# Performance work log

Measured on AMD Instinct MI355X. Metric: run time of the kernel, lower is better.

Reference implementation:

```python
import math
import jax, jax.numpy as jnp
import numpy as np

V = 32000   # vocab_size
NL = 8      # n_layer
NH = 16     # n_head
D = 1024    # n_embd
DH = D // NH
FF = 4 * D
B = 2
L = 1024
EPS = 1e-5


def setup_inputs() -> dict:
    key = jax.random.key(0)
    ks = jax.random.split(key, 10)
    std = 0.02  # matches nn.init.normal_(std=0.02)
    def nrm(k, shape):
        return jax.random.normal(k, shape, jnp.float32) * std
    return {
        "idx": jax.random.randint(ks[0], (B, L), 0, V),
        "tok_emb": nrm(ks[1], (V, D)),
        # per-layer params stacked on leading NL axis (scanned over)
        "ln1_w": jnp.ones((NL, D)), "ln1_b": jnp.zeros((NL, D)),
        "wq": nrm(ks[2], (NL, D, D)), "wk": nrm(ks[3], (NL, D, D)),
        "wv": nrm(ks[4], (NL, D, D)), "wo": nrm(ks[5], (NL, D, D)),
        "ln2_w": jnp.ones((NL, D)), "ln2_b": jnp.zeros((NL, D)),
        "w1": nrm(ks[6], (NL, D, FF)), "b1": jnp.zeros((NL, FF)),
        "w2": nrm(ks[7], (NL, FF, D)), "b2": jnp.zeros((NL, D)),
        "lnf_w": jnp.ones((D,)), "lnf_b": jnp.zeros((D,)),
        "lm_head": nrm(ks[8], (D, V)),
    }


def _sinusoidal_pe(seq_len, dim):
    pos = jnp.arange(seq_len, dtype=jnp.float32)[:, None]
    div = jnp.exp(jnp.arange(0, dim, 2, dtype=jnp.float32) * (-math.log(10000.0) / dim))
    pe = jnp.zeros((seq_len, dim), jnp.float32)
    pe = pe.at[:, 0::2].set(jnp.sin(pos * div))
    pe = pe.at[:, 1::2].set(jnp.cos(pos * div))
    return pe


def _ln(x, w, b):
    m = x.mean(-1, keepdims=True)
    v = ((x - m) ** 2).mean(-1, keepdims=True)
    return (x - m) * jax.lax.rsqrt(v + EPS) * w + b


def reference(idx, tok_emb, ln1_w, ln1_b, wq, wk, wv, wo,
              ln2_w, ln2_b, w1, b1, w2, b2, lnf_w, lnf_b, lm_head):
    b, l = idx.shape
    x = tok_emb[idx] + _sinusoidal_pe(l, tok_emb.shape[1])[None]  # [B,L,D]
    causal = jnp.tril(jnp.ones((l, l), bool))
    scale = 1.0 / math.sqrt(DH)

    def block(x, p):
        l1w, l1b, Wq, Wk, Wv, Wo, l2w, l2b, W1, B1, W2, B2 = p
        h = _ln(x, l1w, l1b)
        def heads(W):  # [B,L,D] -> [B,H,L,DH]
            return (h @ W).reshape(b, l, NH, DH).transpose(0, 2, 1, 3)
        q, k, v = heads(Wq), heads(Wk), heads(Wv)
        att = jnp.einsum('bhqd,bhkd->bhqk', q, k) * scale
        att = jnp.where(causal, att, -jnp.inf)
        att = jax.nn.softmax(att, axis=-1)
        y = jnp.einsum('bhqk,bhkd->bhqd', att, v)
        y = y.transpose(0, 2, 1, 3).reshape(b, l, -1)
        x = x + y @ Wo
        h2 = _ln(x, l2w, l2b)
        x = x + jax.nn.gelu(h2 @ W1 + B1, approximate=False) @ W2 + B2
        return x, None

    x, _ = jax.lax.scan(
        block, x, (ln1_w, ln1_b, wq, wk, wv, wo, ln2_w, ln2_b, w1, b1, w2, b2))
    x = _ln(x, lnf_w, lnf_b)
    return x @ lm_head  # [B,L,V] logits
```

## Files before the change

kernel.cpp:

```cpp
#include <hip/hip_runtime.h>
#include <math.h>

typedef unsigned short u16;
typedef __bf16 bfx8 __attribute__((ext_vector_type(8)));
typedef float f32x4 __attribute__((ext_vector_type(4)));

#define NLAYER  8
#define NHEAD   16
#define DMODEL  1024
#define DHEAD   64
#define DFF     4096
#define NB      2
#define SEQ     1024
#define NVOCAB  32000
#define NTOK    (NB*SEQ)
#define EPSLN   1e-5f
#define VCHUNK  6400
#define NSPLIT  2

__device__ __forceinline__ float bf2f(u16 u) {
  union { unsigned int i; float f; } x; x.i = ((unsigned int)u) << 16; return x.f;
}
__device__ __forceinline__ u16 f2bf(float f) {
  unsigned int x = __float_as_uint(f);
  x += 0x7fffu + ((x >> 16) & 1u);
  return (u16)(x >> 16);
}

#if defined(__has_builtin)
#if __has_builtin(__builtin_amdgcn_global_load_lds)
#define HAVE_GLL 1
#endif
#endif

__device__ __forceinline__ void gll16(const void* g, void* lds_base, int lane) {
#ifdef HAVE_GLL
  __builtin_amdgcn_global_load_lds((const __attribute__((address_space(1))) unsigned int*)g,
                                   (__attribute__((address_space(3))) unsigned int*)lds_base,
                                   16, 0, 0);
  (void)lane;
#else
  *(uint4*)((char*)lds_base + lane * 16) = *(const uint4*)g;
#endif
}

enum { EPI_QKV = 0, EPI_GELU_BIAS = 1, EPI_RESID = 2, EPI_RESID_BIAS = 3, EPI_LOGITS = 4 };

template <int EPI, int BM>
__global__ __launch_bounds__(256) void gemm_bt(
    const u16* __restrict__ A, const u16* __restrict__ Bt,
    const float* __restrict__ bias, u16* __restrict__ outb,
    float* __restrict__ outf, int M, int N, int K, int ldc)
{
  constexpr int ARND = BM / 32;
  constexpr int MF = BM / 32;
  constexpr int ABYTES = BM * 64 * 2;
  constexpr int BBYTES = 128 * 64 * 2;
  __shared__ __align__(16) u16 sA[2][BM * 64];
  __shared__ __align__(16) u16 sB[2][128 * 64];

  const int tid  = threadIdx.x;
  const int w    = tid >> 6;
  const int lane = tid & 63;
  const int l16  = lane & 15;
  const int hi   = lane >> 4;
  const int wm   = w >> 1;
  const int wn   = w & 1;

  const int nwg = gridDim.x;
  const int MB  = M / BM;
  const int orig = blockIdx.x;
  const int xcd = orig & 7, li = orig >> 3;
  const int q = nwg >> 3, r = nwg & 7;
  const int work = (xcd < r ? xcd * (q + 1) : r * (q + 1) + (xcd - r) * q) + li;
  const int m0 = (work % MB) * BM;
  const int n0 = (work / MB) * 128;

  const int srow8 = lane >> 3;
  const int su    = lane & 7;

  const u16* gA[ARND]; const u16* gB[4];
  int laOff[ARND]; int lbOff[4];
#pragma unroll
  for (int r2 = 0; r2 < ARND; r2++) {
    const int row = r2 * 32 + w * 8 + srow8;
    const int gu = su ^ (row & 7);
    gA[r2] = A + (size_t)(m0 + row) * K + gu * 8;
    laOff[r2] = (r2 * 32 + w * 8) * 128;
  }
#pragma unroll
  for (int r2 = 0; r2 < 4; r2++) {
    const int row = r2 * 32 + w * 8 + srow8;
    const int gu = su ^ (row & 7);
    gB[r2] = Bt + (size_t)(n0 + row) * K + gu * 8;
    lbOff[r2] = (r2 * 32 + w * 8) * 128;
  }

  f32x4 acc[MF][4];
#pragma unroll
  for (int i = 0; i < MF; i++)
#pragma unroll
    for (int j = 0; j < 4; j++)
#pragma unroll
      for (int r2 = 0; r2 < 4; r2++) acc[i][j][r2] = 0.0f;

#pragma unroll
  for (int r2 = 0; r2 < ARND; r2++) { gll16(gA[r2], (char*)sA[0] + laOff[r2], lane); gA[r2] += 64; }
#pragma unroll
  for (int r2 = 0; r2 < 4; r2++)    { gll16(gB[r2], (char*)sB[0] + lbOff[r2], lane); gB[r2] += 64; }
  __syncthreads();

  const int NT = K >> 6;
  int cur = 0;
  for (int t = 0; t < NT; ++t) {
    if (t + 1 < NT) {
      char* nA = (char*)sA[0] + (cur ^ 1) * ABYTES;
      char* nB = (char*)sB[0] + (cur ^ 1) * BBYTES;
#pragma unroll
      for (int r2 = 0; r2 < ARND; r2++) { gll16(gA[r2], nA + laOff[r2], lane); gA[r2] += 64; }
#pragma unroll
      for (int r2 = 0; r2 < 4; r2++)    { gll16(gB[r2], nB + lbOff[r2], lane); gB[r2] += 64; }
    }

    const char* cA = (const char*)sA[0] + cur * ABYTES;
    const char* cB = (const char*)sB[0] + cur * BBYTES;
    bfx8 aF[MF][2], bF[4][2];
#pragma unroll
    for (int i = 0; i < MF; i++) {
      const int row = wm * (BM / 2) + i * 16 + l16;
      const int rsw = row & 7;
#pragma unroll
      for (int kk = 0; kk < 2; kk++)
        aF[i][kk] = *(const bfx8*)(cA + row * 128 + ((kk * 4 + hi) ^ rsw) * 16);
    }
#pragma unroll
    for (int j = 0; j < 4; j++) {
      const int row = wn * 64 + j * 16 + l16;
      const int rsw = row & 7;
#pragma unroll
      for (int kk = 0; kk < 2; kk++)
        bF[j][kk] = *(const bfx8*)(cB + row * 128 + ((kk * 4 + hi) ^ rsw) * 16);
    }
#pragma unroll
    for (int kk = 0; kk < 2; kk++)
#pragma unroll
      for (int i = 0; i < MF; i++)
#pragma unroll
        for (int j = 0; j < 4; j++)
          acc[i][j] = __builtin_amdgcn_mfma_f32_16x16x32_bf16(aF[i][kk], bF[j][kk], acc[i][j], 0, 0, 0);
    __syncthreads();
    cur ^= 1;
  }

  const int rbase = m0 + wm * (BM / 2);
  const int cbase = n0 + wn * 64;
#pragma unroll
  for (int i = 0; i < MF; i++) {
#pragma unroll
    for (int j = 0; j < 4; j++) {
      const int gcol = cbase + j * 16 + l16;
      float bv = 0.0f;
      if constexpr (EPI == EPI_GELU_BIAS || EPI == EPI_RESID_BIAS) bv = bias[gcol];
#pragma unroll
      for (int r2 = 0; r2 < 4; r2++) {
        const int grow = rbase + i * 16 + hi * 4 + r2;
        float v = acc[i][j][r2];
        const size_t oi = (size_t)grow * ldc + gcol;
        if constexpr (EPI == EPI_QKV) {
          outb[oi] = f2bf(v);
        } else if constexpr (EPI == EPI_GELU_BIAS) {
          v += bv;
          v = 0.5f * v * (1.0f + erff(v * 0.70710678118654752f));
          outb[oi] = f2bf(v);
        } else if constexpr (EPI == EPI_RESID) {
          outf[oi] += v;
        } else if constexpr (EPI == EPI_RESID_BIAS) {
          outf[oi] += v + bv;
        } else {
          outf[oi] = v;
        }
      }
    }
  }
}

__global__ __launch_bounds__(256) void ln_kernel(
    const float* __restrict__ x, const float* __restrict__ w,
    const float* __restrict__ b, u16* __restrict__ out)
{
  const int row = blockIdx.x;
  const int tid = threadIdx.x;
  const float* xr = x + (size_t)row * DMODEL;
  float4 v = *(const float4*)(xr + tid * 4);
  __shared__ float sbuf[4];
  float s = v.x + v.y + v.z + v.w;
#pragma unroll
  for (int o = 32; o > 0; o >>= 1) s += __shfl_xor(s, o, 64);
  if ((tid & 63) == 0) sbuf[tid >> 6] = s;
  __syncthreads();
  const float mean = (sbuf[0] + sbuf[1] + sbuf[2] + sbuf[3]) * (1.0f / DMODEL);
  __syncthreads();
  float d0 = v.x - mean, d1 = v.y - mean, d2 = v.z - mean, d3 = v.w - mean;
  float qq = d0 * d0 + d1 * d1 + d2 * d2 + d3 * d3;
#pragma unroll
  for (int o = 32; o > 0; o >>= 1) qq += __shfl_xor(qq, o, 64);
  if ((tid & 63) == 0) sbuf[tid >> 6] = qq;
  __syncthreads();
  const float var = (sbuf[0] + sbuf[1] + sbuf[2] + sbuf[3]) * (1.0f / DMODEL);
  const float rstd = rsqrtf(var + EPSLN);
  const int c = tid * 4;
  float dv[4] = {d0, d1, d2, d3};
#pragma unroll
  for (int e = 0; e < 4; e++)
    out[(size_t)row * DMODEL + c + e] = f2bf(dv[e] * rstd * w[c + e] + b[c + e]);
}

__global__ __launch_bounds__(256) void embed_kernel(
    const int* __restrict__ idx, const float* __restrict__ tok, float* __restrict__ x)
{
  const int row = blockIdx.x;
  const int l = row & (SEQ - 1);
  const int t = idx[row];
  const int d = threadIdx.x * 4;
#pragma unroll
  for (int e = 0; e < 4; e++) {
    const int dd = d + e;
    const float freq = expf((float)(dd & ~1) * (-9.210340371976184f / (float)DMODEL));
    const float ang = (float)l * freq;
    const float pe = (dd & 1) ? cosf(ang) : sinf(ang);
    x[(size_t)row * DMODEL + dd] = tok[(size_t)t * DMODEL + dd] + pe;
  }
}

__global__ __launch_bounds__(256) void transpose_b(
    const float* __restrict__ in0, u16* __restrict__ out0, int rows, int cols,
    size_t in_ls, size_t out_ls)
{
  __shared__ float tile[32][33];
  const float* in = in0 + (size_t)blockIdx.z * in_ls;
  u16* out = out0 + (size_t)blockIdx.z * out_ls;
  const int c0 = blockIdx.x * 32, r0 = blockIdx.y * 32;
  const int tx = threadIdx.x & 31, ty = threadIdx.x >> 5;
#pragma unroll
  for (int i = ty; i < 32; i += 8)
    tile[i][tx] = in[(size_t)(r0 + i) * cols + c0 + tx];
  __syncthreads();
#pragma unroll
  for (int i = ty; i < 32; i += 8)
    out[(size_t)(c0 + i) * rows + r0 + tx] = f2bf(tile[tx][i]);
}

__global__ __launch_bounds__(256) void transpose6_kernel(
    const float* __restrict__ wq, const float* __restrict__ wk,
    const float* __restrict__ wv, const float* __restrict__ wo,
    const float* __restrict__ w1, const float* __restrict__ w2,
    u16* __restrict__ wT)
{
  __shared__ float tile[32][33];
  const size_t dd = (size_t)DMODEL * DMODEL, dff = (size_t)DMODEL * DFF;
  const int t = blockIdx.x;
  const float* in; u16* out; int rows, cols, cx, cy;
  if (t < 4096) {
    const int mat = t >> 10, tl = t & 1023;
    in = (mat == 0) ? wq : (mat == 1) ? wk : (mat == 2) ? wv : wo;
    out = wT + (size_t)mat * dd; rows = DMODEL; cols = DMODEL;
    cx = tl & 31; cy = tl >> 5;
  } else if (t < 8192) {
    const int tl = t - 4096;
    in = w1; out = wT + 4 * dd; rows = DMODEL; cols = DFF;
    cx = tl & 127; cy = tl >> 7;
  } else {
    const int tl = t - 8192;
    in = w2; out = wT + 4 * dd + dff; rows = DFF; cols = DMODEL;
    cx = tl & 31; cy = tl >> 5;
  }
  const int c0 = cx * 32, r0 = cy * 32;
  const int tx = threadIdx.x & 31, ty = threadIdx.x >> 5;
#pragma unroll
  for (int i = ty; i < 32; i += 8)
    tile[i][tx] = in[(size_t)(r0 + i) * cols + c0 + tx];
  __syncthreads();
#pragma unroll
  for (int i = ty; i < 32; i += 8)
    out[(size_t)(c0 + i) * rows + r0 + tx] = f2bf(tile[tx][i]);
}

__global__ __launch_bounds__(256) void vtrans_kernel(
    const u16* __restrict__ qkv, u16* __restrict__ vt)
{
  __shared__ u16 tile[32][33];
  const int bh = blockIdx.z;
  const int b = bh >> 4, hh = bh & 15;
  const int l0 = blockIdx.x * 32, d0 = blockIdx.y * 32;
  const int tx = threadIdx.x & 31, ty = threadIdx.x >> 5;
#pragma unroll
  for (int i = ty; i < 32; i += 8)
    tile[i][tx] = qkv[(size_t)(b * SEQ + l0 + i) * (3 * DMODEL) + 2 * DMODEL + hh * DHEAD + d0 + tx];
  __syncthreads();
#pragma unroll
  for (int i = ty; i < 32; i += 8)
    vt[(size_t)(bh * DHEAD + d0 + i) * SEQ + l0 + tx] = tile[tx][i];
}

__device__ __forceinline__ int plds_byte(int row, int col) {
  return row * 128 + ((((col >> 3) ^ (row & 7)) << 3) + (col & 7)) * 2;
}

__global__ __launch_bounds__(64) void attn_partial(
    const u16* __restrict__ qkv, const u16* __restrict__ vt,
    float* __restrict__ opart, float* __restrict__ lpart)
{
  __shared__ __align__(16) u16 p_lds[32 * 64];
  const int lane = threadIdx.x;
  const int l16 = lane & 15, hi = lane >> 4;
  const int qt = blockIdx.x, hh = blockIdx.y;
  const int b = blockIdx.z >> 1, sp = blockIdx.z & 1;
  const int q0 = qt * 32;
  const int T = (q0 + 95) >> 6;
  const int t_lo = (T * sp) >> 1;
  const int t_hi = (T * (sp + 1)) >> 1;

  const u16* qptr = qkv;
  const u16* kptr = qkv + DMODEL;
  const size_t rs3 = 3 * DMODEL;
  const size_t hoff = (size_t)hh * DHEAD;

  bfx8 aQ[2][2];
#pragma unroll
  for (int mt = 0; mt < 2; mt++)
#pragma unroll
    for (int kf = 0; kf < 2; kf++)
      aQ[mt][kf] = *(const bfx8*)&qptr[(size_t)(b * SEQ + q0 + mt * 16 + l16) * rs3 + hoff + kf * 32 + hi * 8];

  f32x4 o[2][4];
  float ssum[2][4];
#pragma unroll
  for (int mt = 0; mt < 2; mt++)
#pragma unroll
    for (int r = 0; r < 4; r++) ssum[mt][r] = 0.0f;
#pragma unroll
  for (int mt = 0; mt < 2; mt++)
#pragma unroll
    for (int dt = 0; dt < 4; dt++)
#pragma unroll
      for (int r = 0; r < 4; r++) o[mt][dt][r] = 0.0f;

  for (int kt = t_lo; kt < t_hi; kt++) {
    const int k0 = kt * 64;
    const bool diag = (kt == T - 1);

    bfx8 bK[4][2];
#pragma unroll
    for (int nt = 0; nt < 4; nt++)
#pragma unroll
      for (int kf = 0; kf < 2; kf++)
        bK[nt][kf] = *(const bfx8*)&kptr[(size_t)(b * SEQ + k0 + nt * 16 + l16) * rs3 + hoff + kf * 32 + hi * 8];

    f32x4 s[2][4];
#pragma unroll
    for (int mt = 0; mt < 2; mt++)
#pragma unroll
      for (int nt = 0; nt < 4; nt++) {
#pragma unroll
        for (int r = 0; r < 4; r++) s[mt][nt][r] = 0.0f;
        s[mt][nt] = __builtin_amdgcn_mfma_f32_16x16x32_bf16(aQ[mt][0], bK[nt][0], s[mt][nt], 0, 0, 0);
        s[mt][nt] = __builtin_amdgcn_mfma_f32_16x16x32_bf16(aQ[mt][1], bK[nt][1], s[mt][nt], 0, 0, 0);
      }

#pragma unroll
    for (int mt = 0; mt < 2; mt++) {
#pragma unroll
      for (int r = 0; r < 4; r++) {
        const int row_l = mt * 16 + hi * 4 + r;
        const int qrow = q0 + row_l;
        float p[4], rsum = 0.0f;
#pragma unroll
        for (int nt = 0; nt < 4; nt++) {
          const float sv = s[mt][nt][r] * 0.125f;
          const bool mask = diag && (k0 + nt * 16 + l16 > qrow);
          p[nt] = mask ? 0.0f : __expf(sv);
          rsum += p[nt];
        }
#pragma unroll
        for (int t = 1; t < 16; t <<= 1) rsum += __shfl_xor(rsum, t, 64);
        ssum[mt][r] += rsum;
#pragma unroll
        for (int nt = 0; nt < 4; nt++)
          *(u16*)((char*)p_lds + plds_byte(row_l, nt * 16 + l16)) = f2bf(p[nt]);
      }
    }
    __syncthreads();

    bfx8 pa[2][2];
#pragma unroll
    for (int mt = 0; mt < 2; mt++) {
      const int row = mt * 16 + l16;
#pragma unroll
      for (int kf = 0; kf < 2; kf++)
        pa[mt][kf] = *(const bfx8*)((const char*)p_lds + row * 128 + (((kf * 4 + hi) ^ (row & 7)) << 4));
    }
    bfx8 bV[4][2];
    const size_t vbase = (size_t)(b * NHEAD + hh) * DHEAD * SEQ;
#pragma unroll
    for (int dt = 0; dt < 4; dt++)
#pragma unroll
      for (int kf = 0; kf < 2; kf++)
        bV[dt][kf] = *(const bfx8*)&vt[vbase + (size_t)(dt * 16 + l16) * SEQ + k0 + kf * 32 + hi * 8];
#pragma unroll
    for (int mt = 0; mt < 2; mt++)
#pragma unroll
      for (int dt = 0; dt < 4; dt++) {
        o[mt][dt] = __builtin_amdgcn_mfma_f32_16x16x32_bf16(pa[mt][0], bV[dt][0], o[mt][dt], 0, 0, 0);
        o[mt][dt] = __builtin_amdgcn_mfma_f32_16x16x32_bf16(pa[mt][1], bV[dt][1], o[mt][dt], 0, 0, 0);
      }
    __syncthreads();
  }

  const size_t pbase = (((size_t)sp * NB + b) * NHEAD + hh) * SEQ + q0;
#pragma unroll
  for (int mt = 0; mt < 2; mt++) {
#pragma unroll
    for (int r = 0; r < 4; r++) {
      const int row_l = mt * 16 + hi * 4 + r;
      const size_t rg = pbase + row_l;
      if (l16 == 0) lpart[rg] = ssum[mt][r];
#pragma unroll
      for (int dt = 0; dt < 4; dt++)
        opart[rg * DHEAD + dt * 16 + l16] = o[mt][dt][r];
    }
  }
}

__global__ __launch_bounds__(256) void attn_combine(
    const float* __restrict__ opart, const float* __restrict__ lpart,
    u16* __restrict__ y)
{
  const int row = blockIdx.x;
  const int b = row >> 10;
  const int l = row & (SEQ - 1);
  const int t = threadIdx.x;
  const int hh = t >> 4;
  const int d0 = (t & 15) * 4;
  const size_t base = ((size_t)b * NHEAD + hh) * SEQ + l;
  const size_t stride = (size_t)NB * NHEAD * SEQ;
  float wsum = 0.0f;
  float4 acc = make_float4(0.f, 0.f, 0.f, 0.f);
#pragma unroll
  for (int i = 0; i < NSPLIT; i++) {
    wsum += lpart[base + i * stride];
    const float4 ov = *(const float4*)&opart[(base + i * stride) * DHEAD + d0];
    acc.x += ov.x; acc.y += ov.y; acc.z += ov.z; acc.w += ov.w;
  }
  const float dn = 1.0f / wsum;
  u16* yp = y + (size_t)row * DMODEL + hh * DHEAD + d0;
  yp[0] = f2bf(acc.x * dn);
  yp[1] = f2bf(acc.y * dn);
  yp[2] = f2bf(acc.z * dn);
  yp[3] = f2bf(acc.w * dn);
}

extern "C" void kernel_launch(void* const* d_in, const int* in_sizes, int n_in,
                              void* d_out, int out_size, void* d_ws, size_t ws_size,
                              hipStream_t stream)
{
  (void)in_sizes; (void)n_in; (void)out_size;
  const int*   idx  = (const int*)d_in[0];
  const float* tok  = (const float*)d_in[1];
  const float* ln1w = (const float*)d_in[2];
  const float* ln1b = (const float*)d_in[3];
  const float* wq   = (const float*)d_in[4];
  const float* wk   = (const float*)d_in[5];
  const float* wv   = (const float*)d_in[6];
  const float* wo   = (const float*)d_in[7];
  const float* ln2w = (const float*)d_in[8];
  const float* ln2b = (const float*)d_in[9];
  const float* w1   = (const float*)d_in[10];
  const float* b1   = (const float*)d_in[11];
  const float* w2   = (const float*)d_in[12];
  const float* b2   = (const float*)d_in[13];
  const float* lnfw = (const float*)d_in[14];
  const float* lnfb = (const float*)d_in[15];
  const float* lmh  = (const float*)d_in[16];
  float* out = (float*)d_out;

  char* ws = (char*)d_ws;
  size_t off = 0;
  auto alloc = [&](size_t bytes) -> void* {
    void* p = ws + off;
    off += (bytes + 255) & ~(size_t)255;
    return p;
  };
  float* x  = (float*)alloc((size_t)NTOK * DMODEL * 4);
  u16* h    = (u16*)alloc((size_t)NTOK * DMODEL * 2);
  u16* qkv  = (u16*)alloc((size_t)NTOK * 3 * DMODEL * 2);
  u16* vtb  = (u16*)alloc((size_t)NTOK * DMODEL * 2);
  u16* yb   = (u16*)alloc((size_t)NTOK * DMODEL * 2);
  u16* ffb  = (u16*)alloc((size_t)NTOK * DFF * 2);
  float* opart = (float*)alloc((size_t)NSPLIT * NB * NHEAD * SEQ * DHEAD * 4);
  float* lpart = (float*)alloc((size_t)NSPLIT * NB * NHEAD * SEQ * 4);

  const size_t dd = (size_t)DMODEL * DMODEL, dff = (size_t)DMODEL * DFF;
  const size_t perLayerElems = 4 * dd + 2 * dff;
  const size_t wT_bytes = perLayerElems * 2;
  const size_t lmhT_bytes = (size_t)NVOCAB * DMODEL * 2;

  u16* wT = (u16*)alloc(wT_bytes);
  const bool full_lmh = (off + lmhT_bytes) <= ws_size;
  u16* lmhT = full_lmh ? (u16*)alloc(lmhT_bytes) : nullptr;

  embed_kernel<<<NTOK, 256, 0, stream>>>(idx, tok, x);

  const int gQKV = (3 * DMODEL / 128) * (NTOK / 128);
  const int gFF1 = (DFF / 128) * (NTOK / 128);
  const int gD64 = (DMODEL / 128) * (NTOK / 64);

  u16* wqT = wT;
  u16* woT = wT + 3 * dd;
  u16* w1T = wT + 4 * dd;
  u16* w2T = w1T + dff;

  for (int layer = 0; layer < NLAYER; layer++) {
    transpose6_kernel<<<12288, 256, 0, stream>>>(
        wq + layer * dd, wk + layer * dd, wv + layer * dd, wo + layer * dd,
        w1 + layer * dff, w2 + layer * dff, wT);

    ln_kernel<<<NTOK, 256, 0, stream>>>(x, ln1w + layer * DMODEL, ln1b + layer * DMODEL, h);
    gemm_bt<EPI_QKV, 128><<<gQKV, 256, 0, stream>>>(h, wqT, nullptr, qkv, nullptr,
                                                    NTOK, 3 * DMODEL, DMODEL, 3 * DMODEL);
    vtrans_kernel<<<dim3(SEQ / 32, DHEAD / 32, NB * NHEAD), 256, 0, stream>>>(qkv, vtb);
    attn_partial<<<dim3(SEQ / 32, NHEAD, NB * NSPLIT), 64, 0, stream>>>(
        qkv, vtb, opart, lpart);
    attn_combine<<<NB * SEQ, 256, 0, stream>>>(opart, lpart, yb);
    gemm_bt<EPI_RESID, 64><<<gD64, 256, 0, stream>>>(yb, woT, nullptr, nullptr, x,
                                                     NTOK, DMODEL, DMODEL, DMODEL);
    ln_kernel<<<NTOK, 256, 0, stream>>>(x, ln2w + layer * DMODEL, ln2b + layer * DMODEL, h);
    gemm_bt<EPI_GELU_BIAS, 128><<<gFF1, 256, 0, stream>>>(h, w1T, b1 + (size_t)layer * DFF, ffb,
                                                          nullptr, NTOK, DFF, DMODEL, DFF);
    gemm_bt<EPI_RESID_BIAS, 64><<<gD64, 256, 0, stream>>>(ffb, w2T, b2 + (size_t)layer * DMODEL,
                                                          nullptr, x, NTOK, DMODEL, DFF, DMODEL);
  }

  ln_kernel<<<NTOK, 256, 0, stream>>>(x, lnfw, lnfb, h);

  if (full_lmh) {
    transpose_b<<<dim3(NVOCAB/32, DMODEL/32, 1), 256, 0, stream>>>(lmh, lmhT, DMODEL, NVOCAB, 0, 0);
    const int gLM = (NVOCAB / 128) * (NTOK / 128);
    gemm_bt<EPI_LOGITS, 128><<<gLM, 256, 0, stream>>>(
        h, lmhT, nullptr, nullptr, out, NTOK, NVOCAB, DMODEL, NVOCAB);
  } else {
    for (int c = 0; c < NVOCAB / VCHUNK; c++) {
      transpose_b<<<dim3(VCHUNK/32, DMODEL/32, 1), 256, 0, stream>>>(
          lmh + (size_t)c * VCHUNK, wT, DMODEL, NVOCAB, 0, 0);
      gemm_bt<EPI_LOGITS, 128><<<(VCHUNK / 128) * (NTOK / 128), 256, 0, stream>>>(
          h, wT, nullptr, nullptr, out + (size_t)c * VCHUNK,
          NTOK, VCHUNK, DMODEL, NVOCAB);
    }
  }
}
```

Measured before the change: 1.915 ms.

## Halve GEMM K-tile, single-pass layernorm, and 64x64 vectorized weight transposes

The GEMM K tile drops from 64 to 32, halving shared memory per block (more resident blocks) but doubling the number of loop iterations and barriers. LayerNorm now computes the sum and sum of squares in one reduction pass, removing one reduction and two barriers at some risk of cancellation in the variance. The weight transpose kernels move to 64x64 tiles with float4 loads and packed 32-bit bf16 stores, cutting block count and memory transactions.

```diff
diff --git a/kernel.cpp b/kernel.cpp
--- a/kernel.cpp
+++ b/kernel.cpp
@@ -52,12 +52,12 @@
     const float* __restrict__ bias, u16* __restrict__ outb,
     float* __restrict__ outf, int M, int N, int K, int ldc)
 {
-  constexpr int ARND = BM / 32;
+  constexpr int ARND = BM / 64;
   constexpr int MF = BM / 32;
-  constexpr int ABYTES = BM * 64 * 2;
-  constexpr int BBYTES = 128 * 64 * 2;
-  __shared__ __align__(16) u16 sA[2][BM * 64];
-  __shared__ __align__(16) u16 sB[2][128 * 64];
+  constexpr int ABYTES = BM * 32 * 2;
+  constexpr int BBYTES = 128 * 32 * 2;
+  __shared__ __align__(16) u16 sA[2][BM * 32];
+  __shared__ __align__(16) u16 sB[2][128 * 32];
 
   const int tid  = threadIdx.x;
   const int w    = tid >> 6;
@@ -76,24 +76,24 @@
   const int m0 = (work % MB) * BM;
   const int n0 = (work / MB) * 128;
 
-  const int srow8 = lane >> 3;
-  const int su    = lane & 7;
-
-  const u16* gA[ARND]; const u16* gB[4];
-  int laOff[ARND]; int lbOff[4];
+  const int srow = lane >> 2;
+  const int su   = lane & 3;
+
+  const u16* gA[ARND]; const u16* gB[2];
+  int laOff[ARND]; int lbOff[2];
 #pragma unroll
   for (int r2 = 0; r2 < ARND; r2++) {
-    const int row = r2 * 32 + w * 8 + srow8;
-    const int gu = su ^ (row & 7);
+    const int row = r2 * 64 + w * 16 + srow;
+    const int gu = su ^ (row & 3);
     gA[r2] = A + (size_t)(m0 + row) * K + gu * 8;
-    laOff[r2] = (r2 * 32 + w * 8) * 128;
-  }
-#pragma unroll
-  for (int r2 = 0; r2 < 4; r2++) {
-    const int row = r2 * 32 + w * 8 + srow8;
-    const int gu = su ^ (row & 7);
+    laOff[r2] = (r2 * 64 + w * 16) * 64;
+  }
+#pragma unroll
+  for (int r2 = 0; r2 < 2; r2++) {
+    const int row = r2 * 64 + w * 16 + srow;
+    const int gu = su ^ (row & 3);
     gB[r2] = Bt + (size_t)(n0 + row) * K + gu * 8;
-    lbOff[r2] = (r2 * 32 + w * 8) * 128;
+    lbOff[r2] = (r2 * 64 + w * 16) * 64;
   }
 
   f32x4 acc[MF][4];
@@ -105,49 +105,41 @@
       for (int r2 = 0; r2 < 4; r2++) acc[i][j][r2] = 0.0f;
 
 #pragma unroll
-  for (int r2 = 0; r2 < ARND; r2++) { gll16(gA[r2], (char*)sA[0] + laOff[r2], lane); gA[r2] += 64; }
-#pragma unroll
-  for (int r2 = 0; r2 < 4; r2++)    { gll16(gB[r2], (char*)sB[0] + lbOff[r2], lane); gB[r2] += 64; }
+  for (int r2 = 0; r2 < ARND; r2++) { gll16(gA[r2], (char*)sA[0] + laOff[r2], lane); gA[r2] += 32; }
+#pragma unroll
+  for (int r2 = 0; r2 < 2; r2++)    { gll16(gB[r2], (char*)sB[0] + lbOff[r2], lane); gB[r2] += 32; }
   __syncthreads();
 
-  const int NT = K >> 6;
+  const int NT = K >> 5;
   int cur = 0;
   for (int t = 0; t < NT; ++t) {
     if (t + 1 < NT) {
       char* nA = (char*)sA[0] + (cur ^ 1) * ABYTES;
       char* nB = (char*)sB[0] + (cur ^ 1) * BBYTES;
 #pragma unroll
-      for (int r2 = 0; r2 < ARND; r2++) { gll16(gA[r2], nA + laOff[r2], lane); gA[r2] += 64; }
-#pragma unroll
-      for (int r2 = 0; r2 < 4; r2++)    { gll16(gB[r2], nB + lbOff[r2], lane); gB[r2] += 64; }
+      for (int r2 = 0; r2 < ARND; r2++) { gll16(gA[r2], nA + laOff[r2], lane); gA[r2] += 32; }
+#pragma unroll
+      for (int r2 = 0; r2 < 2; r2++)    { gll16(gB[r2], nB + lbOff[r2], lane); gB[r2] += 32; }
     }
 
     const char* cA = (const char*)sA[0] + cur * ABYTES;
     const char* cB = (const char*)sB[0] + cur * BBYTES;
-    bfx8 aF[MF][2], bF[4][2];
+    bfx8 aF[MF], bF[4];
 #pragma unroll
     for (int i = 0; i < MF; i++) {
       const int row = wm * (BM / 2) + i * 16 + l16;
-      const int rsw = row & 7;
-#pragma unroll
-      for (int kk = 0; kk < 2; kk++)
-        aF[i][kk] = *(const bfx8*)(cA + row * 128 + ((kk * 4 + hi) ^ rsw) * 16);
+      aF[i] = *(const bfx8*)(cA + row * 64 + ((hi ^ (row & 3)) << 4));
     }
 #pragma unroll
     for (int j = 0; j < 4; j++) {
       const int row = wn * 64 + j * 16 + l16;
-      const int rsw = row & 7;
-#pragma unroll
-      for (int kk = 0; kk < 2; kk++)
-        bF[j][kk] = *(const bfx8*)(cB + row * 128 + ((kk * 4 + hi) ^ rsw) * 16);
-    }
-#pragma unroll
-    for (int kk = 0; kk < 2; kk++)
-#pragma unroll
-      for (int i = 0; i < MF; i++)
-#pragma unroll
-        for (int j = 0; j < 4; j++)
-          acc[i][j] = __builtin_amdgcn_mfma_f32_16x16x32_bf16(aF[i][kk], bF[j][kk], acc[i][j], 0, 0, 0);
+      bF[j] = *(const bfx8*)(cB + row * 64 + ((hi ^ (row & 3)) << 4));
+    }
+#pragma unroll
+    for (int i = 0; i < MF; i++)
+#pragma unroll
+      for (int j = 0; j < 4; j++)
+        acc[i][j] = __builtin_amdgcn_mfma_f32_16x16x32_bf16(aF[i], bF[j], acc[i][j], 0, 0, 0);
     __syncthreads();
     cur ^= 1;
   }
@@ -192,24 +184,18 @@
   const int tid = threadIdx.x;
   const float* xr = x + (size_t)row * DMODEL;
   float4 v = *(const float4*)(xr + tid * 4);
-  __shared__ float sbuf[4];
+  __shared__ float sbuf[4], qbuf[4];
   float s = v.x + v.y + v.z + v.w;
-#pragma unroll
-  for (int o = 32; o > 0; o >>= 1) s += __shfl_xor(s, o, 64);
-  if ((tid & 63) == 0) sbuf[tid >> 6] = s;
+  float ss = v.x * v.x + v.y * v.y + v.z * v.z + v.w * v.w;
+#pragma unroll
+  for (int o = 32; o > 0; o >>= 1) { s += __shfl_xor(s, o, 64); ss += __shfl_xor(ss, o, 64); }
+  if ((tid & 63) == 0) { sbuf[tid >> 6] = s; qbuf[tid >> 6] = ss; }
   __syncthreads();
   const float mean = (sbuf[0] + sbuf[1] + sbuf[2] + sbuf[3]) * (1.0f / DMODEL);
-  __syncthreads();
-  float d0 = v.x - mean, d1 = v.y - mean, d2 = v.z - mean, d3 = v.w - mean;
-  float qq = d0 * d0 + d1 * d1 + d2 * d2 + d3 * d3;
-#pragma unroll
-  for (int o = 32; o > 0; o >>= 1) qq += __shfl_xor(qq, o, 64);
-  if ((tid & 63) == 0) sbuf[tid >> 6] = qq;
-  __syncthreads();
-  const float var = (sbuf[0] + sbuf[1] + sbuf[2] + sbuf[3]) * (1.0f / DMODEL);
-  const float rstd = rsqrtf(var + EPSLN);
+  const float ex2  = (qbuf[0] + qbuf[1] + qbuf[2] + qbuf[3]) * (1.0f / DMODEL);
+  const float rstd = rsqrtf(ex2 - mean * mean + EPSLN);
   const int c = tid * 4;
-  float dv[4] = {d0, d1, d2, d3};
+  float dv[4] = {v.x - mean, v.y - mean, v.z - mean, v.w - mean};
 #pragma unroll
   for (int e = 0; e < 4; e++)
     out[(size_t)row * DMODEL + c + e] = f2bf(dv[e] * rstd * w[c + e] + b[c + e]);
@@ -232,22 +218,36 @@
   }
 }
 
-__global__ __launch_bounds__(256) void transpose_b(
-    const float* __restrict__ in0, u16* __restrict__ out0, int rows, int cols,
-    size_t in_ls, size_t out_ls)
-{
-  __shared__ float tile[32][33];
-  const float* in = in0 + (size_t)blockIdx.z * in_ls;
-  u16* out = out0 + (size_t)blockIdx.z * out_ls;
-  const int c0 = blockIdx.x * 32, r0 = blockIdx.y * 32;
-  const int tx = threadIdx.x & 31, ty = threadIdx.x >> 5;
-#pragma unroll
-  for (int i = ty; i < 32; i += 8)
-    tile[i][tx] = in[(size_t)(r0 + i) * cols + c0 + tx];
+__device__ __forceinline__ void transpose64_body(
+    const float* __restrict__ in, u16* __restrict__ out,
+    int rows, int cols, int c0, int r0)
+{
+  __shared__ float tile[64][65];
+  const int lx = threadIdx.x & 15, ly = threadIdx.x >> 4;
+#pragma unroll
+  for (int ii = 0; ii < 4; ii++) {
+    const int rr = ly + ii * 16;
+    const float4 v = *(const float4*)&in[(size_t)(r0 + rr) * cols + c0 + lx * 4];
+    tile[rr][lx * 4 + 0] = v.x;
+    tile[rr][lx * 4 + 1] = v.y;
+    tile[rr][lx * 4 + 2] = v.z;
+    tile[rr][lx * 4 + 3] = v.w;
+  }
   __syncthreads();
-#pragma unroll
-  for (int i = ty; i < 32; i += 8)
-    out[(size_t)(c0 + i) * rows + r0 + tx] = f2bf(tile[tx][i]);
+  const int sx = threadIdx.x & 31, sy = threadIdx.x >> 5;
+#pragma unroll
+  for (int ii = 0; ii < 8; ii++) {
+    const int cc = sy + ii * 8;
+    const unsigned int a = f2bf(tile[sx * 2][cc]);
+    const unsigned int b = f2bf(tile[sx * 2 + 1][cc]);
+    *(unsigned int*)&out[(size_t)(c0 + cc) * rows + r0 + sx * 2] = a | (b << 16);
+  }
+}
+
+__global__ __launch_bounds__(256) void transpose64_b(
+    const float* __restrict__ in, u16* __restrict__ out, int rows, int cols)
+{
+  transpose64_body(in, out, rows, cols, blockIdx.x * 64, blockIdx.y * 64);
 }
 
 __global__ __launch_bounds__(256) void transpose6_kernel(
@@ -256,33 +256,24 @@
     const float* __restrict__ w1, const float* __restrict__ w2,
     u16* __restrict__ wT)
 {
-  __shared__ float tile[32][33];
   const size_t dd = (size_t)DMODEL * DMODEL, dff = (size_t)DMODEL * DFF;
   const int t = blockIdx.x;
   const float* in; u16* out; int rows, cols, cx, cy;
-  if (t < 4096) {
-    const int mat = t >> 10, tl = t & 1023;
+  if (t < 1024) {
+    const int mat = t >> 8, tl = t & 255;
     in = (mat == 0) ? wq : (mat == 1) ? wk : (mat == 2) ? wv : wo;
     out = wT + (size_t)mat * dd; rows = DMODEL; cols = DMODEL;
-    cx = tl & 31; cy = tl >> 5;
-  } else if (t < 8192) {
-    const int tl = t - 4096;
+    cx = tl & 15; cy = tl >> 4;
+  } else if (t < 2048) {
+    const int tl = t - 1024;
     in = w1; out = wT + 4 * dd; rows = DMODEL; cols = DFF;
-    cx = tl & 127; cy = tl >> 7;
+    cx = tl & 63; cy = tl >> 6;
   } else {
-    const int tl = t - 8192;
+    const int tl = t - 2048;
     in = w2; out = wT + 4 * dd + dff; rows = DFF; cols = DMODEL;
-    cx = tl & 31; cy = tl >> 5;
-  }
-  const int c0 = cx * 32, r0 = cy * 32;
-  const int tx = threadIdx.x & 31, ty = threadIdx.x >> 5;
-#pragma unroll
-  for (int i = ty; i < 32; i += 8)
-    tile[i][tx] = in[(size_t)(r0 + i) * cols + c0 + tx];
-  __syncthreads();
-#pragma unroll
-  for (int i = ty; i < 32; i += 8)
-    out[(size_t)(c0 + i) * rows + r0 + tx] = f2bf(tile[tx][i]);
+    cx = tl & 15; cy = tl >> 4;
+  }
+  transpose64_body(in, out, rows, cols, cx * 64, cy * 64);
 }
 
 __global__ __launch_bounds__(256) void vtrans_kernel(
@@ -520,7 +511,7 @@
   u16* w2T = w1T + dff;
 
   for (int layer = 0; layer < NLAYER; layer++) {
-    transpose6_kernel<<<12288, 256, 0, stream>>>(
+    transpose6_kernel<<<3072, 256, 0, stream>>>(
         wq + layer * dd, wk + layer * dd, wv + layer * dd, wo + layer * dd,
         w1 + layer * dff, w2 + layer * dff, wT);
 
@@ -543,14 +534,14 @@
   ln_kernel<<<NTOK, 256, 0, stream>>>(x, lnfw, lnfb, h);
 
   if (full_lmh) {
-    transpose_b<<<dim3(NVOCAB/32, DMODEL/32, 1), 256, 0, stream>>>(lmh, lmhT, DMODEL, NVOCAB, 0, 0);
+    transpose64_b<<<dim3(NVOCAB / 64, DMODEL / 64), 256, 0, stream>>>(lmh, lmhT, DMODEL, NVOCAB);
     const int gLM = (NVOCAB / 128) * (NTOK / 128);
     gemm_bt<EPI_LOGITS, 128><<<gLM, 256, 0, stream>>>(
         h, lmhT, nullptr, nullptr, out, NTOK, NVOCAB, DMODEL, NVOCAB);
   } else {
     for (int c = 0; c < NVOCAB / VCHUNK; c++) {
-      transpose_b<<<dim3(VCHUNK/32, DMODEL/32, 1), 256, 0, stream>>>(
-          lmh + (size_t)c * VCHUNK, wT, DMODEL, NVOCAB, 0, 0);
+      transpose64_b<<<dim3(VCHUNK / 64, DMODEL / 64), 256, 0, stream>>>(
+          lmh + (size_t)c * VCHUNK, wT, DMODEL, NVOCAB);
       gemm_bt<EPI_LOGITS, 128><<<(VCHUNK / 128) * (NTOK / 128), 256, 0, stream>>>(
           h, wT, nullptr, nullptr, out + (size_t)c * VCHUNK,
           NTOK, VCHUNK, DMODEL, NVOCAB);
```

Result: no change. 1.934 ms (+1.0%).
